# Performance work log

Measured on AMD Instinct MI355X. Metric: run time of the kernel, lower is better.

Reference implementation:

```python
import jax, jax.numpy as jnp
import numpy as np

TEMPERATURE = 0.1
EPS = 1e-08
NEG_INF = -9e15


def setup_inputs() -> dict:
    key = jax.random.key(0)
    k1, k2 = jax.random.split(key)
    B, D = 4096, 256
    z_i = jax.random.normal(k1, (B, D), dtype=jnp.float32)
    z_j = jax.random.normal(k2, (B, D), dtype=jnp.float32)
    mask_positive = jnp.ones((B,), dtype=bool)
    return {"z_i": z_i, "z_j": z_j, "mask_positive": mask_positive}


def reference(z_i, z_j, mask_positive):
    B = z_i.shape[0]
    N = 2 * B
    z = jnp.concatenate([z_i, z_j], axis=0)  # [N, D]
    # cosine similarity: normalize (norms clamped to eps) then GEMM
    norms = jnp.maximum(jnp.linalg.norm(z, axis=1, keepdims=True), EPS)
    zn = z / norms
    sim = jnp.matmul(zn, zn.T) / TEMPERATURE  # [N, N]
    # mask self-similarity on diagonal
    rows = jnp.arange(N)
    sim = sim.at[rows, rows].set(NEG_INF)
    logprob = jax.nn.log_softmax(sim, axis=1)
    # positive of row k is row (k+B) mod N
    positives = jnp.concatenate([jnp.arange(B, N), jnp.arange(0, B)])
    loss_vec = -logprob[rows, positives]  # [N]
    mp = jnp.concatenate([mask_positive, mask_positive])  # [N] bool
    cnt = jnp.sum(mp.astype(jnp.float32))
    total = jnp.sum(jnp.where(mp, loss_vec, 0.0))
    loss = jnp.where(cnt > 0, total / jnp.maximum(cnt, 1.0), 0.0)
    return loss
```

## Files before the change

### kernel.cpp

```cpp
#include <hip/hip_runtime.h>
#include <hip/hip_bf16.h>

#define NTOT   8192
#define BHALF  4096
#define DDIM   256
#define SMOD   16
#define NPART  4
#define MAXSLOT 9
#define EXPSCALE 14.4269504088896341f

typedef __attribute__((ext_vector_type(8))) short bf16x8_t;
typedef __attribute__((ext_vector_type(4))) float f32x4_t;

__device__ inline unsigned short f2bf(float x) {
    __hip_bfloat16 h = __float2bfloat16(x);
    return __builtin_bit_cast(unsigned short, h);
}

__global__ void norm_pair_kernel(const float* __restrict__ zi,
                                 const float* __restrict__ zj,
                                 unsigned short* __restrict__ zn,
                                 float* __restrict__ posdot,
                                 float* __restrict__ s_part) {
    int gtid = blockIdx.x * 256 + threadIdx.x;
    if (gtid < NTOT * NPART) s_part[gtid] = 0.0f;
    int k    = gtid >> 6;
    int lane = gtid & 63;
    float4 vi = reinterpret_cast<const float4*>(zi + (size_t)k * DDIM)[lane];
    float4 vj = reinterpret_cast<const float4*>(zj + (size_t)k * DDIM)[lane];
    float ssi = vi.x*vi.x + vi.y*vi.y + vi.z*vi.z + vi.w*vi.w;
    float ssj = vj.x*vj.x + vj.y*vj.y + vj.z*vj.z + vj.w*vj.w;
    float dot = vi.x*vj.x + vi.y*vj.y + vi.z*vj.z + vi.w*vj.w;
    #pragma unroll
    for (int off = 32; off >= 1; off >>= 1) {
        ssi += __shfl_xor(ssi, off);
        ssj += __shfl_xor(ssj, off);
        dot += __shfl_xor(dot, off);
    }
    float ri = 1.0f / fmaxf(sqrtf(ssi), 1e-8f);
    float rj = 1.0f / fmaxf(sqrtf(ssj), 1e-8f);
    ushort4 oi, oj;
    oi.x = f2bf(vi.x * ri); oi.y = f2bf(vi.y * ri);
    oi.z = f2bf(vi.z * ri); oi.w = f2bf(vi.w * ri);
    oj.x = f2bf(vj.x * rj); oj.y = f2bf(vj.y * rj);
    oj.z = f2bf(vj.z * rj); oj.w = f2bf(vj.w * rj);
    reinterpret_cast<ushort4*>(zn + (size_t)k * DDIM)[lane] = oi;
    reinterpret_cast<ushort4*>(zn + (size_t)(k + BHALF) * DDIM)[lane] = oj;
    if (lane == 0) posdot[k] = dot * ri * rj * 10.0f;
}

__global__ void __launch_bounds__(256, 2)
gemm_sym_kernel(const unsigned short* __restrict__ zn,
                float* __restrict__ s_part) {
    __shared__ unsigned short ldsB[64 * 256];
    __shared__ float colLDS[MAXSLOT][4][64];

    const int tid  = threadIdx.x;
    const int lane = tid & 63;
    const int wv   = tid >> 6;
    const int m    = lane & 15;
    const int quad = lane >> 4;
    const int biA  = blockIdx.x;
    const int s    = blockIdx.y;

    float* rowPart = s_part + (size_t)(s   & (NPART - 1)) * NTOT;
    float* colPart = s_part + (size_t)(biA & (NPART - 1)) * NTOT;

    int slot = 0;
    #pragma unroll
    for (int p = 0; p < 2; ++p) {
        const int bi = p ? (63 - biA) : biA;
        const int R0 = bi << 7;
        const int cs0 = 2 * bi + ((s - 2 * bi) & (SMOD - 1));
        if (cs0 >= 128) continue;

        bf16x8_t afrag[2][8];
        #pragma unroll
        for (int rf = 0; rf < 2; ++rf) {
            const unsigned short* arow = zn + (size_t)(R0 + wv*32 + rf*16 + m) * DDIM;
            #pragma unroll
            for (int kk = 0; kk < 8; ++kk)
                afrag[rf][kk] = *reinterpret_cast<const bf16x8_t*>(arow + kk*32 + quad*8);
        }

        float rowacc[2][4] = {{0.f,0.f,0.f,0.f},{0.f,0.f,0.f,0.f}};

        for (int cs = cs0; cs < 128; cs += SMOD) {
            const int C0 = cs << 6;
            const bool isDiag = ((cs >> 1) == bi);

            __syncthreads();
            #pragma unroll
            for (int t = 0; t < 8; ++t) {
                int ci = t * 256 + tid;
                int r = ci >> 5, c = ci & 31;
                bf16x8_t v = *reinterpret_cast<const bf16x8_t*>(
                                 zn + (size_t)(C0 + r) * DDIM + c * 8);
                *reinterpret_cast<bf16x8_t*>(&ldsB[r * 256 + ((c ^ (r & 7)) << 3)]) = v;
            }
            __syncthreads();

            #pragma unroll
            for (int cf = 0; cf < 4; ++cf) {
                f32x4_t c0 = (f32x4_t){0.f,0.f,0.f,0.f};
                f32x4_t c1 = (f32x4_t){0.f,0.f,0.f,0.f};
                #pragma unroll
                for (int kk = 0; kk < 8; ++kk) {
                    bf16x8_t b = *reinterpret_cast<const bf16x8_t*>(
                        &ldsB[(cf*16 + m) * 256 + (((kk*4 + quad) ^ (m & 7)) << 3)]);
                    c0 = __builtin_amdgcn_mfma_f32_16x16x32_bf16(afrag[0][kk], b, c0, 0, 0, 0);
                    c1 = __builtin_amdgcn_mfma_f32_16x16x32_bf16(afrag[1][kk], b, c1, 0, 0, 0);
                }
                const int gc = C0 + cf*16 + m;
                float colsum = 0.f;
                #pragma unroll
                for (int r = 0; r < 4; ++r) {
                    int gr0 = R0 + wv*32 + quad*4 + r;
                    float e0 = exp2f(c0[r] * EXPSCALE);
                    float e1 = exp2f(c1[r] * EXPSCALE);
                    if (isDiag && gr0 == gc)        e0 = 0.f;
                    if (isDiag && (gr0 + 16) == gc) e1 = 0.f;
                    rowacc[0][r] += e0;
                    rowacc[1][r] += e1;
                    colsum += e0 + e1;
                }
                if (!isDiag) {
                    colsum += __shfl_xor(colsum, 16);
                    colsum += __shfl_xor(colsum, 32);
                    if (quad == 0) colLDS[slot][wv][cf*16 + m] = colsum;
                }
            }
            ++slot;
        }

        #pragma unroll
        for (int rf = 0; rf < 2; ++rf)
            #pragma unroll
            for (int r = 0; r < 4; ++r) {
                float v = rowacc[rf][r];
                v += __shfl_xor(v, 1);
                v += __shfl_xor(v, 2);
                v += __shfl_xor(v, 4);
                v += __shfl_xor(v, 8);
                if (m == 0)
                    atomicAdd(&rowPart[R0 + wv*32 + rf*16 + quad*4 + r], v);
            }
    }

    __syncthreads();

    if (tid < 64) {
        int slot2 = 0;
        #pragma unroll
        for (int p = 0; p < 2; ++p) {
            const int bi = p ? (63 - biA) : biA;
            const int cs0 = 2 * bi + ((s - 2 * bi) & (SMOD - 1));
            if (cs0 >= 128) continue;
            for (int cs = cs0; cs < 128; cs += SMOD) {
                if ((cs >> 1) != bi) {
                    float v = colLDS[slot2][0][tid] + colLDS[slot2][1][tid]
                            + colLDS[slot2][2][tid] + colLDS[slot2][3][tid];
                    atomicAdd(&colPart[(cs << 6) + tid], v);
                }
                ++slot2;
            }
        }
    }
}

__global__ void finalize_kernel(const float* __restrict__ s_part,
                                const float* __restrict__ posdot,
                                const unsigned char* __restrict__ mask,
                                float* __restrict__ out) {
    int tid = threadIdx.x, lane = tid & 63, wv = tid >> 6;
    float tot = 0.f, cnt = 0.f;
    #pragma unroll
    for (int si = 0; si < NTOT / 1024; ++si) {
        int k = si * 1024 + tid;
        int kb = k & (BHALF - 1);
        if (mask[kb] != 0) {
            float sk = s_part[k] + s_part[NTOT + k]
                     + s_part[2*NTOT + k] + s_part[3*NTOT + k];
            tot += __logf(sk) - posdot[kb];
            cnt += 1.f;
        }
    }
    #pragma unroll
    for (int off = 32; off >= 1; off >>= 1) {
        tot += __shfl_xor(tot, off);
        cnt += __shfl_xor(cnt, off);
    }
    __shared__ float st[16], sc[16];
    if (lane == 0) { st[wv] = tot; sc[wv] = cnt; }
    __syncthreads();
    if (tid == 0) {
        float T = 0.f, C = 0.f;
        #pragma unroll
        for (int i = 0; i < 16; ++i) { T += st[i]; C += sc[i]; }
        out[0] = (C > 0.f) ? (T / fmaxf(C, 1.f)) : 0.f;
    }
}

extern "C" void kernel_launch(void* const* d_in, const int* in_sizes, int n_in,
                              void* d_out, int out_size, void* d_ws, size_t ws_size,
                              hipStream_t stream) {
    const float* zi = (const float*)d_in[0];
    const float* zj = (const float*)d_in[1];
    const unsigned char* mask = (const unsigned char*)d_in[2];
    float* out = (float*)d_out;

    unsigned short* zn = (unsigned short*)d_ws;
    float* s_part = (float*)((char*)d_ws + (size_t)NTOT * DDIM * 2);
    float* posdot = s_part + NPART * NTOT;

    norm_pair_kernel<<<dim3(1024), dim3(256), 0, stream>>>(zi, zj, zn, posdot, s_part);
    gemm_sym_kernel<<<dim3(32, SMOD), dim3(256), 0, stream>>>(zn, s_part);
    finalize_kernel<<<dim3(1), dim3(1024), 0, stream>>>(s_part, posdot, mask, out);
}
```

Before: 107.8 us.

## Restructure symmetric GEMM into single-wave blocks with async LDS double buffering

Replaces the 256-thread blocks handling 128-row strips with 4096 single-wave blocks, each owning a 32-row strip and striding over 16-column tiles. B tiles are staged straight into LDS with global_load_lds in two half-K buffers, using explicit vmcnt waits so the next load overlaps the MFMA work. Block-wide __syncthreads is no longer needed. The diagonal tile is now handled by keeping only the strict upper triangle, so the column sums also feed the transposed contributions. In exchange each tile is smaller and every block reloads its A fragments, which adds more atomics and less reuse per block.

Measured after the change: 119.7 us. +11.1%, slower.

```diff
diff --git a/kernel.cpp b/kernel.cpp
--- a/kernel.cpp
+++ b/kernel.cpp
@@ -4,9 +4,8 @@
 #define NTOT   8192
 #define BHALF  4096
 #define DDIM   256
-#define SMOD   16
 #define NPART  4
-#define MAXSLOT 9
+#define MAXSLOT 18
 #define EXPSCALE 14.4269504088896341f
 
 typedef __attribute__((ext_vector_type(8))) short bf16x8_t;
@@ -49,121 +48,150 @@
     if (lane == 0) posdot[k] = dot * ri * rj * 10.0f;
 }
 
-__global__ void __launch_bounds__(256, 2)
+__global__ void __attribute__((amdgpu_flat_work_group_size(64, 64),
+                               amdgpu_waves_per_eu(4, 4)))
 gemm_sym_kernel(const unsigned short* __restrict__ zn,
                 float* __restrict__ s_part) {
-    __shared__ unsigned short ldsB[64 * 256];
-    __shared__ float colLDS[MAXSLOT][4][64];
-
-    const int tid  = threadIdx.x;
-    const int lane = tid & 63;
-    const int wv   = tid >> 6;
+    __shared__ unsigned short ldsA[2048];
+    __shared__ unsigned short ldsB[2048];
+    __shared__ float colLDS[MAXSLOT][16];
+
+    const int lane = threadIdx.x;
     const int m    = lane & 15;
     const int quad = lane >> 4;
-    const int biA  = blockIdx.x;
-    const int s    = blockIdx.y;
-
-    float* rowPart = s_part + (size_t)(s   & (NPART - 1)) * NTOT;
-    float* colPart = s_part + (size_t)(biA & (NPART - 1)) * NTOT;
+    const int wid  = blockIdx.x;
+    const int p    = wid >> 5;
+    const int j    = wid & 31;
+
+    float* rowPart = s_part + (size_t)(j & (NPART - 1)) * NTOT;
+    float* colPart = s_part + (size_t)(p & (NPART - 1)) * NTOT;
+
+#define STAGE(dst, sV, hV) {                                                  \
+    _Pragma("unroll")                                                         \
+    for (int t_ = 0; t_ < 4; ++t_) {                                          \
+        int ci_ = t_ * 64 + lane;                                             \
+        int r_ = ci_ >> 4, c_ = ci_ & 15;                                     \
+        const unsigned short* g_ = zn + (size_t)((sV) * 16 + r_) * DDIM       \
+                                   + (hV) * 128 + ((c_ ^ (r_ & 7)) << 3);     \
+        __builtin_amdgcn_global_load_lds(                                     \
+            (const __attribute__((address_space(1))) unsigned int*)g_,        \
+            (__attribute__((address_space(3))) unsigned int*)((dst) + ci_*8), \
+            16, 0, 0);                                                        \
+    } }
+
+#define HALF(buf, hV) {                                                       \
+    bf16x8_t bfr[4];                                                          \
+    _Pragma("unroll")                                                         \
+    for (int kk_ = 0; kk_ < 4; ++kk_)                                         \
+        bfr[kk_] = *reinterpret_cast<const bf16x8_t*>(                        \
+            (buf) + m * 128 + ((((kk_ << 2) + quad) ^ (m & 7)) << 3));        \
+    _Pragma("unroll")                                                         \
+    for (int kk_ = 0; kk_ < 4; ++kk_) {                                       \
+        acc0 = __builtin_amdgcn_mfma_f32_16x16x32_bf16(                       \
+                   afrag[0][(hV)*4 + kk_], bfr[kk_], acc0, 0, 0, 0);          \
+        acc1 = __builtin_amdgcn_mfma_f32_16x16x32_bf16(                       \
+                   afrag[1][(hV)*4 + kk_], bfr[kk_], acc1, 0, 0, 0);          \
+    } }
 
     int slot = 0;
     #pragma unroll
-    for (int p = 0; p < 2; ++p) {
-        const int bi = p ? (63 - biA) : biA;
-        const int R0 = bi << 7;
-        const int cs0 = 2 * bi + ((s - 2 * bi) & (SMOD - 1));
-        if (cs0 >= 128) continue;
+    for (int ph = 0; ph < 2; ++ph) {
+        const int R    = ph ? (255 - p) : p;
+        const int jj   = ph ? (31 - j) : j;
+        const int smin = 2 * R;
+        int s = smin + ((jj - smin) & 31);
+        if (s >= 512) continue;
 
         bf16x8_t afrag[2][8];
         #pragma unroll
         for (int rf = 0; rf < 2; ++rf) {
-            const unsigned short* arow = zn + (size_t)(R0 + wv*32 + rf*16 + m) * DDIM;
+            const unsigned short* ap =
+                zn + (size_t)((R << 5) + rf * 16 + m) * DDIM + quad * 8;
             #pragma unroll
             for (int kk = 0; kk < 8; ++kk)
-                afrag[rf][kk] = *reinterpret_cast<const bf16x8_t*>(arow + kk*32 + quad*8);
-        }
-
-        float rowacc[2][4] = {{0.f,0.f,0.f,0.f},{0.f,0.f,0.f,0.f}};
-
-        for (int cs = cs0; cs < 128; cs += SMOD) {
-            const int C0 = cs << 6;
-            const bool isDiag = ((cs >> 1) == bi);
-
-            __syncthreads();
+                afrag[rf][kk] = *reinterpret_cast<const bf16x8_t*>(ap + kk * 32);
+        }
+        #pragma unroll
+        for (int rf = 0; rf < 2; ++rf)
             #pragma unroll
-            for (int t = 0; t < 8; ++t) {
-                int ci = t * 256 + tid;
-                int r = ci >> 5, c = ci & 31;
-                bf16x8_t v = *reinterpret_cast<const bf16x8_t*>(
-                                 zn + (size_t)(C0 + r) * DDIM + c * 8);
-                *reinterpret_cast<bf16x8_t*>(&ldsB[r * 256 + ((c ^ (r & 7)) << 3)]) = v;
+            for (int kk = 0; kk < 8; ++kk) {
+                int4 t_ = __builtin_bit_cast(int4, afrag[rf][kk]);
+                asm volatile("" : "+v"(t_.x), "+v"(t_.y), "+v"(t_.z), "+v"(t_.w));
+                afrag[rf][kk] = __builtin_bit_cast(bf16x8_t, t_);
             }
-            __syncthreads();
-
-            #pragma unroll
-            for (int cf = 0; cf < 4; ++cf) {
-                f32x4_t c0 = (f32x4_t){0.f,0.f,0.f,0.f};
-                f32x4_t c1 = (f32x4_t){0.f,0.f,0.f,0.f};
-                #pragma unroll
-                for (int kk = 0; kk < 8; ++kk) {
-                    bf16x8_t b = *reinterpret_cast<const bf16x8_t*>(
-                        &ldsB[(cf*16 + m) * 256 + (((kk*4 + quad) ^ (m & 7)) << 3)]);
-                    c0 = __builtin_amdgcn_mfma_f32_16x16x32_bf16(afrag[0][kk], b, c0, 0, 0, 0);
-                    c1 = __builtin_amdgcn_mfma_f32_16x16x32_bf16(afrag[1][kk], b, c1, 0, 0, 0);
-                }
-                const int gc = C0 + cf*16 + m;
+
+        float ra0[4] = {0.f, 0.f, 0.f, 0.f};
+        float ra1[4] = {0.f, 0.f, 0.f, 0.f};
+
+        STAGE(ldsA, s, 0);
+        for (;;) {
+            STAGE(ldsB, s, 1);
+            asm volatile("s_waitcnt vmcnt(4)" ::: "memory");
+            __builtin_amdgcn_sched_barrier(0);
+            f32x4_t acc0 = (f32x4_t){0.f, 0.f, 0.f, 0.f};
+            f32x4_t acc1 = (f32x4_t){0.f, 0.f, 0.f, 0.f};
+            HALF(ldsA, 0);
+
+            const bool more = (s + 32 < 512);
+            if (more) { STAGE(ldsA, s + 32, 0); }
+            if (more) { asm volatile("s_waitcnt vmcnt(4)" ::: "memory"); }
+            else      { asm volatile("s_waitcnt vmcnt(0)" ::: "memory"); }
+            __builtin_amdgcn_sched_barrier(0);
+            HALF(ldsB, 1);
+
+            {
+                const int gc = s * 16 + m;
+                const bool dg = ((s >> 1) == R);
                 float colsum = 0.f;
                 #pragma unroll
                 for (int r = 0; r < 4; ++r) {
-                    int gr0 = R0 + wv*32 + quad*4 + r;
-                    float e0 = exp2f(c0[r] * EXPSCALE);
-                    float e1 = exp2f(c1[r] * EXPSCALE);
-                    if (isDiag && gr0 == gc)        e0 = 0.f;
-                    if (isDiag && (gr0 + 16) == gc) e1 = 0.f;
-                    rowacc[0][r] += e0;
-                    rowacc[1][r] += e1;
+                    float e0 = exp2f(acc0[r] * EXPSCALE);
+                    float e1 = exp2f(acc1[r] * EXPSCALE);
+                    if (dg) {
+                        int gr0 = (R << 5) + quad * 4 + r;
+                        e0 = (gc > gr0)      ? e0 : 0.f;
+                        e1 = (gc > gr0 + 16) ? e1 : 0.f;
+                    }
+                    ra0[r] += e0;
+                    ra1[r] += e1;
                     colsum += e0 + e1;
                 }
-                if (!isDiag) {
-                    colsum += __shfl_xor(colsum, 16);
-                    colsum += __shfl_xor(colsum, 32);
-                    if (quad == 0) colLDS[slot][wv][cf*16 + m] = colsum;
-                }
+                colsum += __shfl_xor(colsum, 16);
+                colsum += __shfl_xor(colsum, 32);
+                if (quad == 0) colLDS[slot][m] = colsum;
+                ++slot;
             }
-            ++slot;
-        }
-
-        #pragma unroll
-        for (int rf = 0; rf < 2; ++rf)
-            #pragma unroll
-            for (int r = 0; r < 4; ++r) {
-                float v = rowacc[rf][r];
-                v += __shfl_xor(v, 1);
-                v += __shfl_xor(v, 2);
-                v += __shfl_xor(v, 4);
-                v += __shfl_xor(v, 8);
-                if (m == 0)
-                    atomicAdd(&rowPart[R0 + wv*32 + rf*16 + quad*4 + r], v);
+            if (!more) break;
+            s += 32;
+        }
+
+        #pragma unroll
+        for (int r = 0; r < 4; ++r) {
+            float v0 = ra0[r], v1 = ra1[r];
+            v0 += __shfl_xor(v0, 1); v0 += __shfl_xor(v0, 2);
+            v0 += __shfl_xor(v0, 4); v0 += __shfl_xor(v0, 8);
+            v1 += __shfl_xor(v1, 1); v1 += __shfl_xor(v1, 2);
+            v1 += __shfl_xor(v1, 4); v1 += __shfl_xor(v1, 8);
+            if (m == 0) {
+                atomicAdd(&rowPart[(R << 5) + quad * 4 + r], v0);
+                atomicAdd(&rowPart[(R << 5) + 16 + quad * 4 + r], v1);
             }
-    }
-
-    __syncthreads();
-
-    if (tid < 64) {
-        int slot2 = 0;
-        #pragma unroll
-        for (int p = 0; p < 2; ++p) {
-            const int bi = p ? (63 - biA) : biA;
-            const int cs0 = 2 * bi + ((s - 2 * bi) & (SMOD - 1));
-            if (cs0 >= 128) continue;
-            for (int cs = cs0; cs < 128; cs += SMOD) {
-                if ((cs >> 1) != bi) {
-                    float v = colLDS[slot2][0][tid] + colLDS[slot2][1][tid]
-                            + colLDS[slot2][2][tid] + colLDS[slot2][3][tid];
-                    atomicAdd(&colPart[(cs << 6) + tid], v);
-                }
-                ++slot2;
-            }
+        }
+    }
+#undef STAGE
+#undef HALF
+
+    int slot2 = 0;
+    #pragma unroll
+    for (int ph = 0; ph < 2; ++ph) {
+        const int R    = ph ? (255 - p) : p;
+        const int jj   = ph ? (31 - j) : j;
+        const int smin = 2 * R;
+        int s = smin + ((jj - smin) & 31);
+        for (; s < 512; s += 32) {
+            float v = colLDS[slot2][m];
+            if (quad == 0) atomicAdd(&colPart[s * 16 + m], v);
+            ++slot2;
         }
     }
 }
@@ -214,6 +242,6 @@
     float* posdot = s_part + NPART * NTOT;
 
     norm_pair_kernel<<<dim3(1024), dim3(256), 0, stream>>>(zi, zj, zn, posdot, s_part);
-    gemm_sym_kernel<<<dim3(32, SMOD), dim3(256), 0, stream>>>(zn, s_part);
+    gemm_sym_kernel<<<dim3(4096), dim3(64), 0, stream>>>(zn, s_part);
     finalize_kernel<<<dim3(1), dim3(1024), 0, stream>>>(s_part, posdot, mask, out);
 }
```
